# Performance work log

Hardware: AMD Instinct MI355X
Metric: run time of the kernel (lower is better)

Reference implementation:

```python
import jax, jax.numpy as jnp
import numpy as np

DIM = 2048
N_HEADS = 32
N_KV_HEADS = 4
HEAD_DIM = DIM // N_HEADS  # 64


def _rope_tables(T, head_dim, dtype):
    inv_freq = 1.0 / (10000.0 ** (jnp.arange(0, head_dim, 2, dtype=jnp.float32) / head_dim))
    t = jnp.arange(T, dtype=jnp.float32)
    freqs = jnp.einsum('i,j->ij', t, inv_freq)           # [T, head_dim/2]
    emb = jnp.concatenate([freqs, freqs], axis=-1)        # [T, head_dim]
    return jnp.cos(emb).astype(dtype), jnp.sin(emb).astype(dtype)


def _rotate_half(x):
    d = x.shape[-1] // 2
    return jnp.concatenate([-x[..., d:], x[..., :d]], axis=-1)


def setup_inputs() -> dict:
    key = jax.random.key(0)
    kx, kq, kk, kv, ko = jax.random.split(key, 5)
    s = 1.0 / np.sqrt(DIM)
    return {
        'x': jax.random.normal(kx, (2, 2048, DIM), dtype=jnp.float32),
        'wq': jax.random.normal(kq, (DIM, DIM), dtype=jnp.float32) * s,
        'wk': jax.random.normal(kk, (DIM, DIM // 8), dtype=jnp.float32) * s,
        'wv': jax.random.normal(kv, (DIM, DIM // 8), dtype=jnp.float32) * s,
        'wo': jax.random.normal(ko, (DIM, DIM), dtype=jnp.float32) * s,
    }


def reference(x, wq, wk, wv, wo):
    B, T, C = x.shape
    q = (x @ wq).reshape(B, T, N_HEADS, HEAD_DIM).transpose(0, 2, 1, 3)      # [B,H,T,D]
    k = (x @ wk).reshape(B, T, N_KV_HEADS, HEAD_DIM).transpose(0, 2, 1, 3)   # [B,Hkv,T,D]
    v = (x @ wv).reshape(B, T, N_KV_HEADS, HEAD_DIM).transpose(0, 2, 1, 3)

    cos, sin = _rope_tables(T, HEAD_DIM, x.dtype)  # [T,D]
    q = q * cos + _rotate_half(q) * sin
    k = k * cos + _rotate_half(k) * sin

    rep = N_HEADS // N_KV_HEADS
    k = jnp.repeat(k, rep, axis=1)  # [B,H,T,D]
    v = jnp.repeat(v, rep, axis=1)

    scale = 1.0 / np.sqrt(HEAD_DIM)
    scores = jnp.einsum('bhqd,bhkd->bhqk', q, k) * scale
    causal = jnp.tril(jnp.ones((T, T), dtype=bool))
    scores = jnp.where(causal, scores, jnp.finfo(scores.dtype).min)
    attn = jax.nn.softmax(scores, axis=-1)
    out = jnp.einsum('bhqk,bhkd->bhqd', attn, v)
    out = out.transpose(0, 2, 1, 3).reshape(B, T, C)
    return out @ wo
```

## Files before the change

kernel.cpp:

```cpp
#include <hip/hip_runtime.h>
#include <hip/hip_bf16.h>
#include <stdint.h>

#define DIM 2048
#define TSEQ 2048
#define BATCH 2
#define NH 32
#define NKV 4
#define HD 64
#define MROWS (BATCH*TSEQ)
#define NQKV 2560

typedef __attribute__((ext_vector_type(4))) float f32x4;
typedef __attribute__((ext_vector_type(8))) __bf16 bf16x8;
typedef unsigned short ushort_t;

#define GLDS16(g, l) __builtin_amdgcn_global_load_lds( \
    (const __attribute__((address_space(1))) void*)(g), \
    (__attribute__((address_space(3))) void*)(l), 16, 0, 0)

__device__ __forceinline__ float bflo2f(unsigned int w) {
  union { unsigned int i; float f; } c; c.i = w << 16; return c.f;
}
__device__ __forceinline__ unsigned short f2bf(float f) {
  union { float f; unsigned int i; } c; c.f = f;
  unsigned int x = c.i;
  x += 0x7fffu + ((x >> 16) & 1u);
  return (unsigned short)(x >> 16);
}
__device__ __forceinline__ unsigned short f2bf_fast(float f) {
  union { float f; unsigned int i; } c; c.f = f;
  return (unsigned short)((c.i + 0x8000u) >> 16);
}

__global__ void cast_bf16_k(const float* __restrict__ in, ushort_t* __restrict__ out, int n4) {
  const int i = blockIdx.x * 256 + threadIdx.x;
  if (i >= n4) return;
  const float4 v = ((const float4*)in)[i];
  uint2 p;
  p.x = (unsigned int)f2bf(v.x) | ((unsigned int)f2bf(v.y) << 16);
  p.y = (unsigned int)f2bf(v.z) | ((unsigned int)f2bf(v.w) << 16);
  ((uint2*)out)[i] = p;
}

__global__ void transpose_cast_all(const float* __restrict__ wq, const float* __restrict__ wk,
                                   const float* __restrict__ wv, const float* __restrict__ wo,
                                   ushort_t* __restrict__ wtq, ushort_t* __restrict__ woT) {
  __shared__ float tile[32][33];
  const int by = blockIdx.y;
  const float* src; ushort_t* dst; int N, bnb;
  if (by < 64)      { src = wq; dst = wtq;                    N = DIM; bnb = by; }
  else if (by < 72) { src = wk; dst = wtq + (long)DIM  * DIM; N = 256; bnb = by - 64; }
  else if (by < 80) { src = wv; dst = wtq + (long)2304 * DIM; N = 256; bnb = by - 72; }
  else              { src = wo; dst = woT;                    N = DIM; bnb = by - 80; }
  const int bk = blockIdx.x * 32;
  const int bn = bnb * 32;
  const int tx = threadIdx.x & 31;
  const int ty = threadIdx.x >> 5;
#pragma unroll
  for (int p = 0; p < 4; p++) {
    const int r = ty + p * 8;
    tile[r][tx] = src[(long)(bk + r) * N + bn + tx];
  }
  __syncthreads();
#pragma unroll
  for (int p = 0; p < 4; p++) {
    const int r = ty + p * 8;
    dst[(long)(bn + r) * DIM + bk + tx] = f2bf(tile[tx][r]);
  }
}

#define LOG1E4_D32 0.2878231366242557f
#define QSCALE 0.1803368801111243f

__global__ void rope_tab_k(float2* __restrict__ tab) {
  const int i = blockIdx.x * 256 + threadIdx.x;
  const int t = i >> 5, d = i & 31;
  const float ang = (float)t * __expf(-(float)d * LOG1E4_D32);
  float s_, c_;
  __sincosf(ang, &s_, &c_);
  tab[i] = make_float2(c_, s_);
}

template<int EPI>
__global__ __launch_bounds__(256, 2) void gemm_bt(
    const ushort_t* __restrict__ A, const ushort_t* __restrict__ BT,
    int M, int N, int K,
    float* __restrict__ Cf, ushort_t* __restrict__ Cq,
    ushort_t* __restrict__ Ck, ushort_t* __restrict__ Cv,
    const float2* __restrict__ tab)
{
  __shared__ __align__(16) ushort_t As[128][64];
  __shared__ __align__(16) ushort_t Bs[128][64];
  const int tid  = threadIdx.x;
  const int lane = tid & 63;
  const int wid  = tid >> 6;
  const int wm   = wid >> 1, wn = wid & 1;
  const int l8   = lane >> 3;
  const int c8   = (lane & 7) * 8;
  const long abase = (long)blockIdx.x * 128 * K;
  const long bbase = (long)blockIdx.y * 128 * K;
  const int rsel = lane & 15;
  const int koff = (lane >> 4) * 8;
  f32x4 acc[4][4] = {};

  for (int k0 = 0; k0 < K; k0 += 64) {
    __syncthreads();
#pragma unroll
    for (int i = 0; i < 4; i++) {
      const int r0 = wid * 32 + i * 8;
      GLDS16(&A [abase + (long)(r0 + l8) * K + k0 + c8], &As[r0][0]);
      GLDS16(&BT[bbase + (long)(r0 + l8) * K + k0 + c8], &Bs[r0][0]);
    }
    __syncthreads();
#pragma unroll
    for (int kk = 0; kk < 64; kk += 32) {
      bf16x8 af[4], bfr[4];
#pragma unroll
      for (int m = 0; m < 4; m++) af[m]  = *(const bf16x8*)(&As[wm*64 + m*16 + rsel][kk + koff]);
#pragma unroll
      for (int n = 0; n < 4; n++) bfr[n] = *(const bf16x8*)(&Bs[wn*64 + n*16 + rsel][kk + koff]);
#pragma unroll
      for (int m = 0; m < 4; m++)
#pragma unroll
        for (int n = 0; n < 4; n++)
          acc[m][n] = __builtin_amdgcn_mfma_f32_16x16x32_bf16(af[m], bfr[n], acc[m][n], 0, 0, 0);
    }
  }

  const int rbase = blockIdx.x * 128 + wm * 64 + (lane >> 4) * 4;
  const int l15e  = lane & 15;

  if (EPI == 1) {
    const int cbase = blockIdx.y * 128 + wn * 64 + l15e;
#pragma unroll
    for (int m = 0; m < 4; m++)
#pragma unroll
      for (int n = 0; n < 4; n++) {
        const int gn = cbase + n * 16;
#pragma unroll
        for (int j = 0; j < 4; j++)
          Cf[(long)(rbase + m * 16 + j) * N + gn] = acc[m][n][j];
      }
  } else {
    const int colbase = blockIdx.y * 128 + wn * 64;
    if (colbase >= DIM + 256) {
#pragma unroll
      for (int m = 0; m < 4; m++) {
        const int gm0 = rbase + m * 16;
        const int b = gm0 >> 11;
        const int t = gm0 & (TSEQ - 1);
#pragma unroll
        for (int n = 0; n < 4; n++) {
          const int x = colbase + n * 16 + l15e - DIM;
          const int hkv = (x >> 6) & 3;
          const int d = x & 63;
          uint2 pk;
          pk.x = (unsigned int)f2bf(acc[m][n][0]) | ((unsigned int)f2bf(acc[m][n][1]) << 16);
          pk.y = (unsigned int)f2bf(acc[m][n][2]) | ((unsigned int)f2bf(acc[m][n][3]) << 16);
          *(uint2*)(&Cv[((long)(b * NKV + hkv) * HD + d) * TSEQ + t]) = pk;
        }
      }
    } else {
      const bool isQ = (colbase < DIM);
      const int hkv = (colbase - DIM) >> 6;
#pragma unroll
      for (int m = 0; m < 4; m++) {
#pragma unroll
        for (int j = 0; j < 4; j++) {
          const int gm = rbase + m * 16 + j;
          const int t = gm & (TSEQ - 1);
          const int b = gm >> 11;
          const float2 cs0 = tab[t * 32 + l15e];
          const float2 cs1 = tab[t * 32 + 16 + l15e];
          const float v0 = acc[m][0][j], v1 = acc[m][1][j];
          const float v2 = acc[m][2][j], v3 = acc[m][3][j];
          const float r0 = v0 * cs0.x - v2 * cs0.y;
          const float r2 = v2 * cs0.x + v0 * cs0.y;
          const float r1 = v1 * cs1.x - v3 * cs1.y;
          const float r3 = v3 * cs1.x + v1 * cs1.y;
          if (isQ) {
            const long base = (long)gm * DIM + colbase + l15e;
            Cq[base]      = f2bf(r0 * QSCALE);
            Cq[base + 16] = f2bf(r1 * QSCALE);
            Cq[base + 32] = f2bf(r2 * QSCALE);
            Cq[base + 48] = f2bf(r3 * QSCALE);
          } else {
            const long base = ((long)(b * NKV + hkv) * TSEQ + t) * HD + l15e;
            Ck[base]      = f2bf(r0);
            Ck[base + 16] = f2bf(r1);
            Ck[base + 32] = f2bf(r2);
            Ck[base + 48] = f2bf(r3);
          }
        }
      }
    }
  }
}

__global__ __launch_bounds__(512, 4) void attn_mfma(
    const ushort_t* __restrict__ q, const ushort_t* __restrict__ k,
    const ushort_t* __restrict__ vt, ushort_t* __restrict__ o)
{
  __shared__ __align__(16) ushort_t Ks[2][64][64];
  __shared__ __align__(16) ushort_t Vs[2][64][64];

  const int tid  = threadIdx.x;
  const int lane = tid & 63;
  const int wid  = tid >> 6;
  const int l15  = lane & 15;
  const int lg   = lane >> 4;
  const int od   = lg & 1;
  const int hi   = lg >> 1;
  const int sw   = l15 & 7;

  const int bh  = blockIdx.x & 63;
  const int pq  = blockIdx.x >> 6;
  const int qtA = 15 - pq;
  const int qtB = pq;
  const int h   = bh & (NH - 1);
  const int b   = bh >> 5;
  const int hkv = h >> 3;
  const int qA0 = qtA * 128 + wid * 16;
  const int qB0 = qtB * 128 + wid * 16;

  bf16x8 qfA0, qfA1, qfB0, qfB1;
  {
    const ushort_t* qp = q + ((long)(b * TSEQ) + qA0 + l15) * DIM + h * 64 + lg * 8;
    qfA0 = *(const bf16x8*)(qp);
    qfA1 = *(const bf16x8*)(qp + 32);
    const ushort_t* qp2 = q + ((long)(b * TSEQ) + qB0 + l15) * DIM + h * 64 + lg * 8;
    qfB0 = *(const bf16x8*)(qp2);
    qfB1 = *(const bf16x8*)(qp2 + 32);
  }

  const ushort_t* kb_ = k  + (long)(b * NKV + hkv) * TSEQ * HD;
  const ushort_t* vb_ = vt + (long)(b * NKV + hkv) * HD * TSEQ;

  float lA = 0.f, lB = 0.f;
  f32x4 oA[4] = {}, oB[4] = {};

  const int srow = tid >> 3;
  const int sgc  = (tid & 7) * 8;
  const int slc  = (((tid & 7) ^ (srow & 7))) * 8;

  const int gv0 = ((0 + 2 * od + hi) ^ sw) * 8;
  const int gv1 = ((4 + 2 * od + hi) ^ sw) * 8;

  const int nkv = 2 * (qtA + 1);

  *(uint4*)(&Ks[0][srow][slc]) = *(const uint4*)(&kb_[(long)srow * HD + sgc]);
  *(uint4*)(&Vs[0][srow][slc]) = *(const uint4*)(&vb_[(long)srow * TSEQ + sgc]);
  int cur = 0;

#define PROC_TILE(QF0, QF1, OO, LL, Q0) \
  if (kb0 <= (Q0) + 15) { \
    f32x4 st[4] = {}; \
    _Pragma("unroll") \
    for (int kt = 0; kt < 4; kt++) { \
      const bf16x8 kf0 = *(const bf16x8*)(&Ks[cur][kt * 16 + l15][((0 + lg) ^ sw) * 8]); \
      st[kt] = __builtin_amdgcn_mfma_f32_16x16x32_bf16(kf0, QF0, st[kt], 0, 0, 0); \
      const bf16x8 kf1 = *(const bf16x8*)(&Ks[cur][kt * 16 + l15][((4 + lg) ^ sw) * 8]); \
      st[kt] = __builtin_amdgcn_mfma_f32_16x16x32_bf16(kf1, QF1, st[kt], 0, 0, 0); \
    } \
    if (kb0 + 63 > (Q0)) { \
      const int qg = (Q0) + l15; \
      _Pragma("unroll") \
      for (int kt = 0; kt < 4; kt++) { \
        const int kg0 = kb0 + kt * 16 + lg * 4; \
        _Pragma("unroll") \
        for (int j = 0; j < 4; j++) { \
          if (kg0 + j > qg) st[kt][j] = -1e30f; \
        } \
      } \
    } \
    unsigned int u00, u01, u10, u11, u20, u21, u30, u31; \
    PACK_KT(0, u00, u01, LL) \
    PACK_KT(1, u10, u11, LL) \
    PACK_KT(2, u20, u21, LL) \
    PACK_KT(3, u30, u31, LL) \
    const unsigned int r00 = __shfl_xor((int)(od ? u00 : u10), 16, 64); \
    const unsigned int r01 = __shfl_xor((int)(od ? u01 : u11), 16, 64); \
    const unsigned int r10 = __shfl_xor((int)(od ? u20 : u30), 16, 64); \
    const unsigned int r11 = __shfl_xor((int)(od ? u21 : u31), 16, 64); \
    union { unsigned int u[4]; bf16x8 v; } T0, T1; \
    T0.u[0] = od ? r00 : u00;  T0.u[1] = od ? r01 : u01; \
    T0.u[2] = od ? u10 : r00;  T0.u[3] = od ? u11 : r01; \
    T1.u[0] = od ? r10 : u20;  T1.u[1] = od ? r11 : u21; \
    T1.u[2] = od ? u30 : r10;  T1.u[3] = od ? u31 : r11; \
    _Pragma("unroll") \
    for (int nt = 0; nt < 4; nt++) { \
      const bf16x8 vf0 = *(const bf16x8*)(&Vs[cur][nt * 16 + l15][gv0]); \
      OO[nt] = __builtin_amdgcn_mfma_f32_16x16x32_bf16(T0.v, vf0, OO[nt], 0, 0, 0); \
    } \
    _Pragma("unroll") \
    for (int nt = 0; nt < 4; nt++) { \
      const bf16x8 vf1 = *(const bf16x8*)(&Vs[cur][nt * 16 + l15][gv1]); \
      OO[nt] = __builtin_amdgcn_mfma_f32_16x16x32_bf16(T1.v, vf1, OO[nt], 0, 0, 0); \
    } \
  }

#define PACK_KT(KT, UA, UB, LL) { \
    const float p0 = exp2f(st[KT][0]); \
    const float p1 = exp2f(st[KT][1]); \
    const float p2 = exp2f(st[KT][2]); \
    const float p3 = exp2f(st[KT][3]); \
    LL += (p0 + p1) + (p2 + p3); \
    asm("v_cvt_pk_bf16_f32 %0, %1, %2" : "=v"(UA) : "v"(p0), "v"(p1)); \
    asm("v_cvt_pk_bf16_f32 %0, %1, %2" : "=v"(UB) : "v"(p2), "v"(p3)); \
  }

  for (int kbv = 0; kbv < nkv; kbv++) {
    const int kb0 = kbv * 64;
    const bool pf = (kbv + 1 < nkv);
    uint4 kr = {}, vr = {};
    if (pf) {
      kr = *(const uint4*)(&kb_[(long)(kb0 + 64 + srow) * HD + sgc]);
      vr = *(const uint4*)(&vb_[(long)srow * TSEQ + kb0 + 64 + sgc]);
    }
    asm volatile("s_waitcnt lgkmcnt(0)\n\ts_barrier" ::: "memory");

    PROC_TILE(qfA0, qfA1, oA, lA, qA0)
    PROC_TILE(qfB0, qfB1, oB, lB, qB0)

    if (pf) {
      *(uint4*)(&Ks[cur ^ 1][srow][slc]) = kr;
      *(uint4*)(&Vs[cur ^ 1][srow][slc]) = vr;
    }
    cur ^= 1;
  }
#undef PROC_TILE
#undef PACK_KT

  {
    float lc = lA;
    lc += __shfl_xor(lc, 16, 64);
    lc += __shfl_xor(lc, 32, 64);
    const long orow = (long)(b * TSEQ) + qA0;
#pragma unroll
    for (int j = 0; j < 4; j++) {
      const float inv = 1.f / __shfl(lc, (lane & 48) | (lg * 4 + j), 64);
#pragma unroll
      for (int nt = 0; nt < 4; nt++)
        o[(orow + lg * 4 + j) * DIM + h * 64 + nt * 16 + l15] = f2bf_fast(oA[nt][j] * inv);
    }
  }
  {
    float lc = lB;
    lc += __shfl_xor(lc, 16, 64);
    lc += __shfl_xor(lc, 32, 64);
    const long orow = (long)(b * TSEQ) + qB0;
#pragma unroll
    for (int j = 0; j < 4; j++) {
      const float inv = 1.f / __shfl(lc, (lane & 48) | (lg * 4 + j), 64);
#pragma unroll
      for (int nt = 0; nt < 4; nt++)
        o[(orow + lg * 4 + j) * DIM + h * 64 + nt * 16 + l15] = f2bf_fast(oB[nt][j] * inv);
    }
  }
}

extern "C" void kernel_launch(void* const* d_in, const int* in_sizes, int n_in,
                              void* d_out, int out_size, void* d_ws, size_t ws_size,
                              hipStream_t stream) {
  const float* x  = (const float*)d_in[0];
  const float* wq = (const float*)d_in[1];
  const float* wk = (const float*)d_in[2];
  const float* wv = (const float*)d_in[3];
  const float* wo = (const float*)d_in[4];
  float* out = (float*)d_out;

  ushort_t* ws = (ushort_t*)d_ws;
  const long NXB = (long)MROWS * DIM;
  ushort_t* xb   = ws;
  ushort_t* wtq  = xb  + NXB;
  ushort_t* woT  = wtq + (long)NQKV * DIM;
  ushort_t* qws  = woT + (long)DIM * DIM;
  ushort_t* kws  = qws + NXB;
  ushort_t* vtws = kws + (long)BATCH * NKV * TSEQ * HD;
  ushort_t* aws  = vtws + (long)BATCH * NKV * TSEQ * HD;
  float2*   tab  = (float2*)(aws + NXB);

  cast_bf16_k<<<(int)(NXB / 1024), 256, 0, stream>>>(x, xb, (int)(NXB / 4));
  transpose_cast_all<<<dim3(64, 144), 256, 0, stream>>>(wq, wk, wv, wo, wtq, woT);
  rope_tab_k<<<256, 256, 0, stream>>>(tab);

  gemm_bt<0><<<dim3(32, 20), 256, 0, stream>>>(xb, wtq, MROWS, NQKV, DIM,
                                               nullptr, qws, kws, vtws, tab);

  attn_mfma<<<BATCH * NH * 8, 512, 0, stream>>>(qws, kws, vtws, aws);

  gemm_bt<1><<<dim3(32, 16), 256, 0, stream>>>(aws, woT, MROWS, DIM, DIM,
                                               out, nullptr, nullptr, nullptr, nullptr);
}
```

Baseline: 200.2 us.

## Halve attention block size to 64-query tiles and add MFMA priority hints

The attention kernel moves from 512-thread blocks covering 128-query tiles to 256-thread blocks covering 64-query tiles, doubling the grid. The paired causal scheduling (tile 31-pq with tile pq) is kept. Each thread now stages two 16-byte chunks per K/V row. s_setprio is raised around the MFMA sections so that matrix work gets issue priority over the softmax/VALU phases of other waves. The aim is better load balance and occupancy across CUs, at the cost of more K/V reloads per query row and more barriers per unit of work.

Result: no change. 202.8 us (+1.3%).

```diff
diff --git a/kernel.cpp b/kernel.cpp
--- a/kernel.cpp
+++ b/kernel.cpp
@@ -198,7 +198,7 @@
   }
 }
 
-__global__ __launch_bounds__(512, 4) void attn_mfma(
+__global__ __launch_bounds__(256, 4) void attn_mfma(
     const ushort_t* __restrict__ q, const ushort_t* __restrict__ k,
     const ushort_t* __restrict__ vt, ushort_t* __restrict__ o)
 {
@@ -216,13 +216,13 @@
 
   const int bh  = blockIdx.x & 63;
   const int pq  = blockIdx.x >> 6;
-  const int qtA = 15 - pq;
+  const int qtA = 31 - pq;
   const int qtB = pq;
   const int h   = bh & (NH - 1);
   const int b   = bh >> 5;
   const int hkv = h >> 3;
-  const int qA0 = qtA * 128 + wid * 16;
-  const int qB0 = qtB * 128 + wid * 16;
+  const int qA0 = qtA * 64 + wid * 16;
+  const int qB0 = qtB * 64 + wid * 16;
 
   bf16x8 qfA0, qfA1, qfB0, qfB1;
   {
@@ -240,22 +240,37 @@
   float lA = 0.f, lB = 0.f;
   f32x4 oA[4] = {}, oB[4] = {};
 
-  const int srow = tid >> 3;
-  const int sgc  = (tid & 7) * 8;
-  const int slc  = (((tid & 7) ^ (srow & 7))) * 8;
+  const int srow = tid >> 2;
+  const int sgc  = (tid & 3) * 16;
+  const int g0   = 2 * (tid & 3);
+  const int slc0 = ((g0    ) ^ (srow & 7)) * 8;
+  const int slc1 = ((g0 + 1) ^ (srow & 7)) * 8;
 
   const int gv0 = ((0 + 2 * od + hi) ^ sw) * 8;
   const int gv1 = ((4 + 2 * od + hi) ^ sw) * 8;
 
-  const int nkv = 2 * (qtA + 1);
-
-  *(uint4*)(&Ks[0][srow][slc]) = *(const uint4*)(&kb_[(long)srow * HD + sgc]);
-  *(uint4*)(&Vs[0][srow][slc]) = *(const uint4*)(&vb_[(long)srow * TSEQ + sgc]);
+  const int nkv = qtA + 1;
+
+  *(uint4*)(&Ks[0][srow][slc0]) = *(const uint4*)(&kb_[(long)srow * HD + sgc]);
+  *(uint4*)(&Ks[0][srow][slc1]) = *(const uint4*)(&kb_[(long)srow * HD + sgc + 8]);
+  *(uint4*)(&Vs[0][srow][slc0]) = *(const uint4*)(&vb_[(long)srow * TSEQ + sgc]);
+  *(uint4*)(&Vs[0][srow][slc1]) = *(const uint4*)(&vb_[(long)srow * TSEQ + sgc + 8]);
   int cur = 0;
+
+#define PACK_KT(KT, UA, UB, LL) { \
+    const float p0 = exp2f(st[KT][0]); \
+    const float p1 = exp2f(st[KT][1]); \
+    const float p2 = exp2f(st[KT][2]); \
+    const float p3 = exp2f(st[KT][3]); \
+    LL += (p0 + p1) + (p2 + p3); \
+    asm("v_cvt_pk_bf16_f32 %0, %1, %2" : "=v"(UA) : "v"(p0), "v"(p1)); \
+    asm("v_cvt_pk_bf16_f32 %0, %1, %2" : "=v"(UB) : "v"(p2), "v"(p3)); \
+  }
 
 #define PROC_TILE(QF0, QF1, OO, LL, Q0) \
   if (kb0 <= (Q0) + 15) { \
     f32x4 st[4] = {}; \
+    __builtin_amdgcn_s_setprio(1); \
     _Pragma("unroll") \
     for (int kt = 0; kt < 4; kt++) { \
       const bf16x8 kf0 = *(const bf16x8*)(&Ks[cur][kt * 16 + l15][((0 + lg) ^ sw) * 8]); \
@@ -263,6 +278,7 @@
       const bf16x8 kf1 = *(const bf16x8*)(&Ks[cur][kt * 16 + l15][((4 + lg) ^ sw) * 8]); \
       st[kt] = __builtin_amdgcn_mfma_f32_16x16x32_bf16(kf1, QF1, st[kt], 0, 0, 0); \
     } \
+    __builtin_amdgcn_s_setprio(0); \
     if (kb0 + 63 > (Q0)) { \
       const int qg = (Q0) + l15; \
       _Pragma("unroll") \
@@ -288,6 +304,7 @@
     T0.u[2] = od ? u10 : r00;  T0.u[3] = od ? u11 : r01; \
     T1.u[0] = od ? r10 : u20;  T1.u[1] = od ? r11 : u21; \
     T1.u[2] = od ? u30 : r10;  T1.u[3] = od ? u31 : r11; \
+    __builtin_amdgcn_s_setprio(1); \
     _Pragma("unroll") \
     for (int nt = 0; nt < 4; nt++) { \
       const bf16x8 vf0 = *(const bf16x8*)(&Vs[cur][nt * 16 + l15][gv0]); \
@@ -298,25 +315,18 @@
       const bf16x8 vf1 = *(const bf16x8*)(&Vs[cur][nt * 16 + l15][gv1]); \
       OO[nt] = __builtin_amdgcn_mfma_f32_16x16x32_bf16(T1.v, vf1, OO[nt], 0, 0, 0); \
     } \
-  }
-
-#define PACK_KT(KT, UA, UB, LL) { \
-    const float p0 = exp2f(st[KT][0]); \
-    const float p1 = exp2f(st[KT][1]); \
-    const float p2 = exp2f(st[KT][2]); \
-    const float p3 = exp2f(st[KT][3]); \
-    LL += (p0 + p1) + (p2 + p3); \
-    asm("v_cvt_pk_bf16_f32 %0, %1, %2" : "=v"(UA) : "v"(p0), "v"(p1)); \
-    asm("v_cvt_pk_bf16_f32 %0, %1, %2" : "=v"(UB) : "v"(p2), "v"(p3)); \
+    __builtin_amdgcn_s_setprio(0); \
   }
 
   for (int kbv = 0; kbv < nkv; kbv++) {
     const int kb0 = kbv * 64;
     const bool pf = (kbv + 1 < nkv);
-    uint4 kr = {}, vr = {};
+    uint4 kr0 = {}, kr1 = {}, vr0 = {}, vr1 = {};
     if (pf) {
-      kr = *(const uint4*)(&kb_[(long)(kb0 + 64 + srow) * HD + sgc]);
-      vr = *(const uint4*)(&vb_[(long)srow * TSEQ + kb0 + 64 + sgc]);
+      kr0 = *(const uint4*)(&kb_[(long)(kb0 + 64 + srow) * HD + sgc]);
+      kr1 = *(const uint4*)(&kb_[(long)(kb0 + 64 + srow) * HD + sgc + 8]);
+      vr0 = *(const uint4*)(&vb_[(long)srow * TSEQ + kb0 + 64 + sgc]);
+      vr1 = *(const uint4*)(&vb_[(long)srow * TSEQ + kb0 + 64 + sgc + 8]);
     }
     asm volatile("s_waitcnt lgkmcnt(0)\n\ts_barrier" ::: "memory");
 
@@ -324,8 +334,10 @@
     PROC_TILE(qfB0, qfB1, oB, lB, qB0)
 
     if (pf) {
-      *(uint4*)(&Ks[cur ^ 1][srow][slc]) = kr;
-      *(uint4*)(&Vs[cur ^ 1][srow][slc]) = vr;
+      *(uint4*)(&Ks[cur ^ 1][srow][slc0]) = kr0;
+      *(uint4*)(&Ks[cur ^ 1][srow][slc1]) = kr1;
+      *(uint4*)(&Vs[cur ^ 1][srow][slc0]) = vr0;
+      *(uint4*)(&Vs[cur ^ 1][srow][slc1]) = vr1;
     }
     cur ^= 1;
   }
@@ -388,7 +400,7 @@
   gemm_bt<0><<<dim3(32, 20), 256, 0, stream>>>(xb, wtq, MROWS, NQKV, DIM,
                                                nullptr, qws, kws, vtws, tab);
 
-  attn_mfma<<<BATCH * NH * 8, 512, 0, stream>>>(qws, kws, vtws, aws);
+  attn_mfma<<<BATCH * NH * 16, 256, 0, stream>>>(qws, kws, vtws, aws);
 
   gemm_bt<1><<<dim3(32, 16), 256, 0, stream>>>(aws, woT, MROWS, DIM, DIM,
                                                out, nullptr, nullptr, nullptr, nullptr);
```
